# Kernel optimization log

Hardware: AMD Instinct MI355X
Metric: run time of the kernel (lower is better)

## Reference

```python
import jax, jax.numpy as jnp
import numpy as np


def _conv(x, w, b, pad):
    o = jax.lax.conv_general_dilated(x, w, (1, 1), [(pad, pad), (pad, pad)],
                                     dimension_numbers=('NCHW', 'OIHW', 'NCHW'))
    return o + b[None, :, None, None]


def _prelu(x, a):
    return jnp.where(x >= 0, x, a * x)


def _bn(x, g, b):
    # training-mode BatchNorm2d (biased variance, eps=1e-5)
    m = jnp.mean(x, axis=(0, 2, 3), keepdims=True)
    v = jnp.var(x, axis=(0, 2, 3), keepdims=True)
    return (x - m) * jax.lax.rsqrt(v + 1e-5) * g[None, :, None, None] + b[None, :, None, None]


def _maxpool2(x):
    return jax.lax.reduce_window(x, -jnp.inf, jax.lax.max, (1, 1, 2, 2), (1, 1, 2, 2), 'VALID')


def _up2(x):
    # bilinear upsample x2, align_corners=True
    B, C, H, W = x.shape
    Ho, Wo = 2 * H, 2 * W
    ys = jnp.arange(Ho, dtype=x.dtype) * ((H - 1) / (Ho - 1))
    xs = jnp.arange(Wo, dtype=x.dtype) * ((W - 1) / (Wo - 1))
    y0 = jnp.floor(ys).astype(jnp.int32)
    y1 = jnp.minimum(y0 + 1, H - 1)
    wy = (ys - y0.astype(x.dtype))[:, None]
    x0 = jnp.floor(xs).astype(jnp.int32)
    x1 = jnp.minimum(x0 + 1, W - 1)
    wx = xs - x0.astype(x.dtype)
    rows = x[:, :, y0, :] * (1 - wy) + x[:, :, y1, :] * wy  # [B,C,Ho,W]
    return rows[:, :, :, x0] * (1 - wx) + rows[:, :, :, x1] * wx


def _dyn_conv(x, w):
    # per-sample dynamic conv: x [B,1,H,W], w [B,Cout,k,k], pad = k//2 - 1
    # fused as a single grouped conv (groups = B) instead of B*Cout tiny launches
    B, Cout, k, _ = w.shape
    pad = k // 2 - 1
    xi = x.reshape(1, B, x.shape[2], x.shape[3])
    wi = w.reshape(B * Cout, 1, k, k)
    o = jax.lax.conv_general_dilated(xi, wi, (1, 1), [(pad, pad), (pad, pad)],
                                     dimension_numbers=('NCHW', 'OIHW', 'NCHW'),
                                     feature_group_count=B)
    return o.reshape(B, Cout, o.shape[2], o.shape[3])


def _double(x, w1, b1, w2, b2, a1, a2):
    return _prelu(_conv(_prelu(_conv(x, w1, b1, 1), a1), w2, b2, 1), a2)


def _forward(x, w, c1_w, c1_b, d2_w1, d2_b1, d2_w2, d2_b2, d3_w1, d3_b1, d3_w2, d3_b2,
             d4_w1, d4_b1, d4_w2, d4_b2, u3_w1, u3_b1, u3_w2, u3_b2, u2_w1, u2_b1,
             u2_w2, u2_b2, u1_w1, u1_b1, u1_w2, u1_b2, last_w, last_b,
             bn1_g, bn1_b, bn2_g, bn2_b, bn3_g, bn3_b, bn4_g, bn4_b, prelu_a):
    c1 = _prelu(_dyn_conv(x, w), prelu_a[0])          # [B,32,H-1,W-1]
    c1 = _prelu(_conv(c1, c1_w, c1_b, 2), prelu_a[1])  # 4x4 pad 2 -> [B,32,H,W]
    c1 = _bn(c1, bn1_g, bn1_b)
    h = _maxpool2(c1)
    c2 = _bn(_double(h, d2_w1, d2_b1, d2_w2, d2_b2, prelu_a[2], prelu_a[3]), bn2_g, bn2_b)
    h = _maxpool2(c2)
    c3 = _bn(_double(h, d3_w1, d3_b1, d3_w2, d3_b2, prelu_a[4], prelu_a[5]), bn3_g, bn3_b)
    h = _maxpool2(c3)
    h = _bn(_double(h, d4_w1, d4_b1, d4_w2, d4_b2, prelu_a[6], prelu_a[7]), bn4_g, bn4_b)
    h = jnp.concatenate([_up2(h), c3], axis=1)  # 512+256
    h = _double(h, u3_w1, u3_b1, u3_w2, u3_b2, prelu_a[8], prelu_a[9])
    h = jnp.concatenate([_up2(h), c2], axis=1)  # 256+128
    h = _double(h, u2_w1, u2_b1, u2_w2, u2_b2, prelu_a[10], prelu_a[11])
    h = jnp.concatenate([_up2(h), c1], axis=1)  # 128+32
    h = _double(h, u1_w1, u1_b1, u1_w2, u1_b2, prelu_a[12], prelu_a[13])
    return _conv(h, last_w, last_b, 0)


def setup_inputs() -> dict:
    key = jax.random.key(0)
    ks = iter(jax.random.split(key, 32))
    d = {}
    d['x'] = jax.random.normal(next(ks), (8, 1, 256, 256), jnp.float32)
    d['w'] = jax.random.normal(next(ks), (8, 32, 8, 8), jnp.float32) * 0.1
    wspecs = [('c1_w', (32, 32, 4, 4)), ('d2_w1', (128, 32, 3, 3)), ('d2_w2', (128, 128, 3, 3)),
              ('d3_w1', (256, 128, 3, 3)), ('d3_w2', (256, 256, 3, 3)),
              ('d4_w1', (512, 256, 3, 3)), ('d4_w2', (512, 512, 3, 3)),
              ('u3_w1', (256, 768, 3, 3)), ('u3_w2', (256, 256, 3, 3)),
              ('u2_w1', (128, 384, 3, 3)), ('u2_w2', (128, 128, 3, 3)),
              ('u1_w1', (32, 160, 3, 3)), ('u1_w2', (32, 32, 3, 3)), ('last_w', (1, 32, 1, 1))]
    for name, shp in wspecs:
        d[name] = jax.random.normal(next(ks), shp, jnp.float32) * 0.05
        d[name.replace('_w', '_b')] = jnp.zeros((shp[0],), jnp.float32)
    for name, c in [('bn1', 32), ('bn2', 128), ('bn3', 256), ('bn4', 512)]:
        d[name + '_g'] = jnp.ones((c,), jnp.float32)
        d[name + '_b'] = jnp.zeros((c,), jnp.float32)
    d['prelu_a'] = jnp.full((14,), 0.25, jnp.float32)
    return d


def reference(x, w, c1_w, c1_b, d2_w1, d2_b1, d2_w2, d2_b2, d3_w1, d3_b1, d3_w2, d3_b2,
              d4_w1, d4_b1, d4_w2, d4_b2, u3_w1, u3_b1, u3_w2, u3_b2, u2_w1, u2_b1,
              u2_w2, u2_b2, u1_w1, u1_b1, u1_w2, u1_b2, last_w, last_b,
              bn1_g, bn1_b, bn2_g, bn2_b, bn3_g, bn3_b, bn4_g, bn4_b, prelu_a):
    return _forward(x, w, c1_w, c1_b, d2_w1, d2_b1, d2_w2, d2_b2, d3_w1, d3_b1,
                    d3_w2, d3_b2, d4_w1, d4_b1, d4_w2, d4_b2, u3_w1, u3_b1, u3_w2,
                    u3_b2, u2_w1, u2_b1, u2_w2, u2_b2, u1_w1, u1_b1, u1_w2, u1_b2,
                    last_w, last_b, bn1_g, bn1_b, bn2_g, bn2_b, bn3_g, bn3_b,
                    bn4_g, bn4_b, prelu_a)
```

## Files before the change

kernel.cpp:

```cpp
#include <hip/hip_runtime.h>
#include <hip/hip_bf16.h>
#include <cstddef>


typedef _Float16 h16;
typedef __attribute__((ext_vector_type(8))) _Float16 h16x8;
typedef __attribute__((ext_vector_type(4))) float f32x4;
union F8 { uint4 u; h16x8 h; };
union UH { unsigned u; h16 h[2]; };

__device__ __forceinline__ float h2f(unsigned short s) {
    union { h16 h; unsigned short s; } c; c.s = s; return (float)c.h;
}
__device__ __forceinline__ unsigned short f2h(float f) {
    union { h16 h; unsigned short s; } c; c.h = (h16)f; return c.s;
}
__device__ __forceinline__ unsigned pack2(float a, float b) {
    return (unsigned)f2h(a) | ((unsigned)f2h(b) << 16);
}
__device__ __forceinline__ void up8(const uint4& v, float* f) {
    f[0]=h2f(v.x&0xffff); f[1]=h2f(v.x>>16);
    f[2]=h2f(v.y&0xffff); f[3]=h2f(v.y>>16);
    f[4]=h2f(v.z&0xffff); f[5]=h2f(v.z>>16);
    f[6]=h2f(v.w&0xffff); f[7]=h2f(v.w>>16);
}

__global__ void k_pack(const float* __restrict__ w, h16* __restrict__ pw,
                       int I, int T, int OB)
{
    int i8 = blockIdx.x * 64 + threadIdx.x;
    if (i8 >= (I >> 3)) return;
    int t = blockIdx.y, o = blockIdx.z;
    int ob = o / OB, om = o - ob * OB;
    int mt = om >> 4, m16 = om & 15;
    int chunk = i8 >> 2, quad = i8 & 3;
    int lane = quad * 16 + m16;
    int nch = I >> 5;
    size_t grp = ((((size_t)ob * T + t) * nch + chunk) * (OB >> 4) + mt) * 64 + lane;
    const float* src = w + ((size_t)o * I + i8 * 8) * T + t;
    h16* d = pw + grp * 8;
#pragma unroll
    for (int j = 0; j < 8; ++j) d[j] = (h16)src[(size_t)j * T];
}

template<int KH, int KW, int PAD, bool UPS, int MT>
__global__ __launch_bounds__(256, 2) void k_conv_mfma(
    const h16* __restrict__ src1, int C1n, int H1, int W1,
    const h16* __restrict__ src2, int C2n,
    int Hin, int Win, int Ho, int Wo,
    const h16* __restrict__ PW, const float* __restrict__ bias,
    const float* __restrict__ pa, int aidx,
    h16* __restrict__ out, int Cout)
{
    constexpr int WINH = 8 + KH - 1, WINW = 32 + KW - 1;
    constexpr int NPIX = WINH * WINW;
    constexpr int NIT  = NPIX * 4;
    constexpr int MAXIT = (NIT + 255) / 256;
    constexpr int TAPS = KH * KW;
    __shared__ unsigned short lds[2][NPIX * 36];

    const int tid = threadIdx.x;
    const int lane = tid & 63, wv = tid >> 6;
    const int quad = lane >> 4, m16 = lane & 15;
    const int nCb = Cout / (16 * MT);
    const int b  = blockIdx.z / nCb, cb = blockIdx.z % nCb;
    const int x0 = blockIdx.x * 32, y0 = blockIdx.y * 8;
    const int Cin = C1n + C2n;
    const int nch = Cin >> 5;
    const int co_base = cb * (16 * MT);
    const int srcH = UPS ? Hin : H1;
    const int srcW = UPS ? Win : W1;

    int lof[MAXIT];
    int g1[MAXIT];
    int fl[MAXIT];
    unsigned fyfx[MAXIT];
    int g2[MAXIT];

    const float ry = UPS ? (float)(H1 - 1) / (float)(Hin - 1) : 0.f;
    const float rx = UPS ? (float)(W1 - 1) / (float)(Win - 1) : 0.f;
    const int W1C = UPS ? W1 * C1n : 0;

#pragma unroll
    for (int it = 0; it < MAXIT; ++it) {
        int i = tid + it * 256;
        if (i >= NIT) { lof[it] = -1; g1[it] = -1; g2[it] = -1; fl[it] = 0; fyfx[it] = 0; continue; }
        int p = i >> 2, q = i & 3;
        int wy = p / WINW, wx = p - wy * WINW;
        int yy = y0 - PAD + wy, xx = x0 - PAD + wx;
        lof[it] = p * 36 + q * 8;
        bool val = (unsigned)yy < (unsigned)srcH && (unsigned)xx < (unsigned)srcW;
        if (UPS) {
            fl[it] = 0; fyfx[it] = 0; g1[it] = -1; g2[it] = -1;
            if (val) {
                float ys = yy * ry, xs = xx * rx;
                int yl0 = (int)ys, xl0 = (int)xs;
                float fy = ys - (float)yl0, fx = xs - (float)xl0;
                g1[it] = ((b * H1 + yl0) * W1 + xl0) * C1n + q * 8;
                fl[it] = (yl0 < H1 - 1 ? 1 : 0) | (xl0 < W1 - 1 ? 2 : 0);
                fyfx[it] = pack2(fy, fx);
                g2[it] = ((b * Hin + yy) * Win + xx) * C2n + q * 8;
            }
        } else {
            fl[it] = 0; fyfx[it] = 0; g2[it] = -1;
            g1[it] = val ? ((b * H1 + yy) * W1 + xx) * C1n + q * 8 : -1;
        }
    }

    f32x4 acc[MT][4];
#pragma unroll
    for (int i = 0; i < MT; ++i)
#pragma unroll
        for (int j = 0; j < 4; ++j) acc[i][j] = (f32x4){0.f, 0.f, 0.f, 0.f};

    auto stage = [&](int c0, unsigned short* buf) {
        if (UPS && c0 < C1n) {
#pragma unroll
            for (int it = 0; it < MAXIT; ++it) {
                int lo = lof[it];
                if (lo < 0) continue;
                uint2 lo8 = {0u, 0u}, hi8 = {0u, 0u};
                int g = g1[it];
                if (g >= 0) {
                    const h16* p00 = src1 + g + c0;
                    int oy = (fl[it] & 1) ? W1C : 0;
                    int ox = (fl[it] & 2) ? C1n : 0;
                    F8 v00, v01, v10, v11;
                    v00.u = *(const uint4*)(p00);
                    v01.u = *(const uint4*)(p00 + ox);
                    v10.u = *(const uint4*)(p00 + oy);
                    v11.u = *(const uint4*)(p00 + oy + ox);
                    UH t; t.u = fyfx[it];
                    h16 fy = t.h[0], fx = t.h[1];
                    h16x8 r0 = v00.h + (v10.h - v00.h) * fy;
                    h16x8 r1 = v01.h + (v11.h - v01.h) * fy;
                    F8 rr; rr.h = r0 + (r1 - r0) * fx;
                    lo8 = make_uint2(rr.u.x, rr.u.y);
                    hi8 = make_uint2(rr.u.z, rr.u.w);
                }
                *(uint2*)&buf[lo] = lo8;
                *(uint2*)&buf[lo + 4] = hi8;
            }
        } else if (UPS) {
            int cs = c0 - C1n;
#pragma unroll
            for (int it = 0; it < MAXIT; ++it) {
                int lo = lof[it];
                if (lo < 0) continue;
                uint4 v = {0u, 0u, 0u, 0u};
                int g = g2[it];
                if (g >= 0) v = *(const uint4*)(src2 + g + cs);
                *(uint2*)&buf[lo] = make_uint2(v.x, v.y);
                *(uint2*)&buf[lo + 4] = make_uint2(v.z, v.w);
            }
        } else {
#pragma unroll
            for (int it = 0; it < MAXIT; ++it) {
                int lo = lof[it];
                if (lo < 0) continue;
                uint4 v = {0u, 0u, 0u, 0u};
                int g = g1[it];
                if (g >= 0) v = *(const uint4*)(src1 + g + c0);
                *(uint2*)&buf[lo] = make_uint2(v.x, v.y);
                *(uint2*)&buf[lo + 4] = make_uint2(v.z, v.w);
            }
        }
    };

    const uint4* PW4 = (const uint4*)PW;
    auto sweep = [&](int ci, const unsigned short* buf) {
        size_t abase = (((size_t)cb * TAPS) * nch + ci) * (MT * 64) + lane;
        const size_t astep = (size_t)nch * (MT * 64);
#pragma unroll
        for (int kx = 0; kx < KW; ++kx) {
            F8 a[KH][MT];
#pragma unroll
            for (int ky = 0; ky < KH; ++ky)
#pragma unroll
                for (int mt = 0; mt < MT; ++mt)
                    a[ky][mt].u = PW4[abase + (size_t)(ky * KW + kx) * astep + mt * 64];
#pragma unroll
            for (int wr = 0; wr < 2 + KH - 1; ++wr) {
#pragma unroll
                for (int cg = 0; cg < 2; ++cg) {
                    int row = (wv << 1) + wr;
                    int col = (cg << 4) + m16;
                    int li = (row * WINW + col + kx) * 36 + quad * 8;
                    F8 bf;
                    ((uint2*)&bf)[0] = *(const uint2*)&buf[li];
                    ((uint2*)&bf)[1] = *(const uint2*)&buf[li + 4];
#pragma unroll
                    for (int ky = 0; ky < KH; ++ky) {
                        int ntr = wr - ky;
                        if (ntr < 0 || ntr > 1) continue;
                        int nt = (ntr << 1) + cg;
#pragma unroll
                        for (int mt = 0; mt < MT; ++mt)
                            acc[mt][nt] = __builtin_amdgcn_mfma_f32_16x16x32_f16(
                                a[ky][mt].h, bf.h, acc[mt][nt], 0, 0, 0);
                    }
                }
            }
        }
    };

    stage(0, lds[0]);
    __syncthreads();
    for (int ci = 0; ci < nch; ++ci) {
        int p = ci & 1;
        if (ci + 1 < nch) stage((ci + 1) << 5, lds[p ^ 1]);
        sweep(ci, lds[p]);
        __syncthreads();
    }

    const float alpha = pa[aidx];
#pragma unroll
    for (int mt = 0; mt < MT; ++mt) {
        int co = co_base + mt * 16 + quad * 4;
        float4 bi = *(const float4*)(bias + co);
#pragma unroll
        for (int nt = 0; nt < 4; ++nt) {
            int y = y0 + (wv << 1) + (nt >> 1);
            int x = x0 + ((nt & 1) << 4) + m16;
            float v0 = acc[mt][nt][0] + bi.x;
            float v1 = acc[mt][nt][1] + bi.y;
            float v2 = acc[mt][nt][2] + bi.z;
            float v3 = acc[mt][nt][3] + bi.w;
            v0 = v0 >= 0.f ? v0 : alpha * v0;
            v1 = v1 >= 0.f ? v1 : alpha * v1;
            v2 = v2 >= 0.f ? v2 : alpha * v2;
            v3 = v3 >= 0.f ? v3 : alpha * v3;
            uint2 r; r.x = pack2(v0, v1); r.y = pack2(v2, v3);
            *(uint2*)(out + ((size_t)((b * Ho + y) * Wo + x)) * Cout + co) = r;
        }
    }
}

__global__ __launch_bounds__(256) void k_dynconv(
    const float* __restrict__ x,
    const float* __restrict__ w,
    const float* __restrict__ pa,
    h16* __restrict__ out)
{
    __shared__ float wl[2048];
    int b = blockIdx.y;
    for (int j = threadIdx.x; j < 2048; j += 256) {
        int t = j >> 5, co = j & 31;
        wl[j] = w[((size_t)(b * 32 + co)) * 64 + t];
    }
    __syncthreads();
    int idx = blockIdx.x * 256 + threadIdx.x;
    if (idx >= 65025) return;
    int py = idx / 255, px = idx - py * 255;
    float acc[32];
#pragma unroll
    for (int c = 0; c < 32; ++c) acc[c] = 0.f;
    const float* xp = x + (size_t)b * 65536;
#pragma unroll
    for (int ky = 0; ky < 8; ++ky) {
        int iy = py + ky - 3;
        if ((unsigned)iy >= 256u) continue;
        const float* row = xp + iy * 256;
#pragma unroll
        for (int kx = 0; kx < 8; ++kx) {
            int ix = px + kx - 3;
            if ((unsigned)ix >= 256u) continue;
            float v = row[ix];
            const float4* wr = (const float4*)&wl[(ky * 8 + kx) * 32];
#pragma unroll
            for (int cg = 0; cg < 8; ++cg) {
                float4 wv = wr[cg];
                acc[cg*4+0] += v * wv.x; acc[cg*4+1] += v * wv.y;
                acc[cg*4+2] += v * wv.z; acc[cg*4+3] += v * wv.w;
            }
        }
    }
    float a = pa[0];
    h16* op = out + ((size_t)(b * 65025 + idx)) * 32;
#pragma unroll
    for (int cg = 0; cg < 4; ++cg) {
        float v[8];
#pragma unroll
        for (int k = 0; k < 8; ++k) {
            float t = acc[cg * 8 + k];
            v[k] = t >= 0.f ? t : a * t;
        }
        uint4 r;
        r.x = pack2(v[0], v[1]); r.y = pack2(v[2], v[3]);
        r.z = pack2(v[4], v[5]); r.w = pack2(v[6], v[7]);
        *(uint4*)(op + cg * 8) = r;
    }
}

__global__ __launch_bounds__(256) void k_pool(
    const h16* __restrict__ in, h16* __restrict__ out,
    int Hin, int Win, int C, int lc8, int lwo, int count)
{
    int idx = blockIdx.x * 256 + threadIdx.x;
    if (idx >= count) return;
    int b = blockIdx.y;
    int c8 = idx & ((1 << lc8) - 1);
    int t  = idx >> lc8;
    int ox = t & ((1 << lwo) - 1);
    int oy = t >> lwo;
    const h16* p = in + ((size_t)((b * Hin + oy * 2) * Win + ox * 2)) * C + c8 * 8;
    uint4 v00 = *(const uint4*)p;
    uint4 v01 = *(const uint4*)(p + C);
    uint4 v10 = *(const uint4*)(p + (size_t)Win * C);
    uint4 v11 = *(const uint4*)(p + (size_t)Win * C + C);
    float a[8], bb[8], c[8], d[8];
    up8(v00, a); up8(v01, bb); up8(v10, c); up8(v11, d);
    uint4 r;
    float m[8];
#pragma unroll
    for (int k = 0; k < 8; ++k) m[k] = fmaxf(fmaxf(a[k], bb[k]), fmaxf(c[k], d[k]));
    r.x = pack2(m[0], m[1]); r.y = pack2(m[2], m[3]);
    r.z = pack2(m[4], m[5]); r.w = pack2(m[6], m[7]);
    int Wo = 1 << lwo;
    *(uint4*)(out + ((size_t)((b * (Hin >> 1) + oy) * Wo + ox)) * C + c8 * 8) = r;
}

__global__ __launch_bounds__(256) void k_bnstats(
    const h16* __restrict__ x, int C, int N, float* __restrict__ sums)
{
    __shared__ float ls[1024];
    for (int j = threadIdx.x; j < 2 * C; j += 256) ls[j] = 0.f;
    __syncthreads();
    int start = blockIdx.x * 256 + threadIdx.x;
    int stride = gridDim.x * 256;
    int c = start & (C - 1);
    float s = 0.f, q = 0.f;
    for (int i = start; i < N; i += stride) {
        float v = h2f(((const unsigned short*)x)[i]);
        s += v; q += v * v;
    }
    atomicAdd(&ls[c], s);
    atomicAdd(&ls[C + c], q);
    __syncthreads();
    for (int j = threadIdx.x; j < 2 * C; j += 256) atomicAdd(&sums[j], ls[j]);
}

__global__ void k_bnfin(
    const float* __restrict__ sums, const float* __restrict__ g,
    const float* __restrict__ bta, int C, float invN, float* __restrict__ sc)
{
    int c = threadIdx.x;
    if (c >= C) return;
    float mean = sums[c] * invN;
    float var  = sums[C + c] * invN - mean * mean;
    float s    = g[c] / sqrtf(var + 1e-5f);
    sc[c]      = s;
    sc[C + c]  = bta[c] - mean * s;
}

__global__ __launch_bounds__(256) void k_bnapply(
    h16* __restrict__ x, int C, int N8, const float* __restrict__ sc)
{
    __shared__ float ls[1024];
    for (int j = threadIdx.x; j < 2 * C; j += 256) ls[j] = sc[j];
    __syncthreads();
    int idx = blockIdx.x * 256 + threadIdx.x;
    if (idx >= N8) return;
    int cb = (idx << 3) & (C - 1);
    h16* p = x + (size_t)idx * 8;
    uint4 v = *(const uint4*)p;
    float f[8];
    up8(v, f);
    uint4 r;
    float o[8];
#pragma unroll
    for (int k = 0; k < 8; ++k) o[k] = f[k] * ls[cb + k] + ls[C + cb + k];
    r.x = pack2(o[0], o[1]); r.y = pack2(o[2], o[3]);
    r.z = pack2(o[4], o[5]); r.w = pack2(o[6], o[7]);
    *(uint4*)p = r;
}

__global__ __launch_bounds__(256) void k_final(
    const h16* __restrict__ in, const float* __restrict__ w,
    const float* __restrict__ bias, float* __restrict__ out)
{
    int idx = blockIdx.x * 256 + threadIdx.x;
    if (idx >= 524288) return;
    const h16* p = in + (size_t)idx * 32;
    float acc = bias[0];
#pragma unroll
    for (int cg = 0; cg < 4; ++cg) {
        uint4 v = *(const uint4*)(p + cg * 8);
        float f[8];
        up8(v, f);
#pragma unroll
        for (int k = 0; k < 8; ++k) acc += f[k] * w[cg * 8 + k];
    }
    out[idx] = acc;
}

extern "C" void kernel_launch(void* const* d_in, const int* in_sizes, int n_in,
                              void* d_out, int out_size, void* d_ws, size_t ws_size,
                              hipStream_t stream)
{
    const float* x      = (const float*)d_in[0];
    const float* w      = (const float*)d_in[1];
    const float* c1_w   = (const float*)d_in[2];
    const float* c1_b   = (const float*)d_in[3];
    const float* d2_w1  = (const float*)d_in[4];
    const float* d2_b1  = (const float*)d_in[5];
    const float* d2_w2  = (const float*)d_in[6];
    const float* d2_b2  = (const float*)d_in[7];
    const float* d3_w1  = (const float*)d_in[8];
    const float* d3_b1  = (const float*)d_in[9];
    const float* d3_w2  = (const float*)d_in[10];
    const float* d3_b2  = (const float*)d_in[11];
    const float* d4_w1  = (const float*)d_in[12];
    const float* d4_b1  = (const float*)d_in[13];
    const float* d4_w2  = (const float*)d_in[14];
    const float* d4_b2  = (const float*)d_in[15];
    const float* u3_w1  = (const float*)d_in[16];
    const float* u3_b1  = (const float*)d_in[17];
    const float* u3_w2  = (const float*)d_in[18];
    const float* u3_b2  = (const float*)d_in[19];
    const float* u2_w1  = (const float*)d_in[20];
    const float* u2_b1  = (const float*)d_in[21];
    const float* u2_w2  = (const float*)d_in[22];
    const float* u2_b2  = (const float*)d_in[23];
    const float* u1_w1  = (const float*)d_in[24];
    const float* u1_b1  = (const float*)d_in[25];
    const float* u1_w2  = (const float*)d_in[26];
    const float* u1_b2  = (const float*)d_in[27];
    const float* last_w = (const float*)d_in[28];
    const float* last_b = (const float*)d_in[29];
    const float* bn1_g  = (const float*)d_in[30];
    const float* bn1_b  = (const float*)d_in[31];
    const float* bn2_g  = (const float*)d_in[32];
    const float* bn2_b  = (const float*)d_in[33];
    const float* bn3_g  = (const float*)d_in[34];
    const float* bn3_b  = (const float*)d_in[35];
    const float* bn4_g  = (const float*)d_in[36];
    const float* bn4_b  = (const float*)d_in[37];
    const float* pa     = (const float*)d_in[38];
    float* out = (float*)d_out;

    h16* A0 = (h16*)d_ws;
    h16* C1 = A0;
    h16* C2 = A0 + 16777216;
    h16* C3 = A0 + 33554432;
    h16* A  = A0 + 41943040;
    h16* B  = A0 + 58720256;
    h16* PWb= A0 + 75497472;
    float* SUMS = (float*)(A0 + 83126272);
    float* SC   = SUMS + 1024;
    size_t need = (size_t)83126272 * 2 + 8192;
    if (ws_size < need) return;

    h16* pw_c1   = PWb;
    h16* pw_d2w1 = PWb + 16384;
    h16* pw_d2w2 = PWb + 53248;
    h16* pw_d3w1 = PWb + 200704;
    h16* pw_d3w2 = PWb + 495616;
    h16* pw_d4w1 = PWb + 1085440;
    h16* pw_d4w2 = PWb + 2265088;
    h16* pw_u3w1 = PWb + 4624384;
    h16* pw_u3w2 = PWb + 6393856;
    h16* pw_u2w1 = PWb + 6983680;
    h16* pw_u2w2 = PWb + 7426048;
    h16* pw_u1w1 = PWb + 7573504;
    h16* pw_u1w2 = PWb + 7619584;

    dim3 blk(256);

    auto pack = [&](const float* src, h16* dst, int I, int T, int O, int OB) {
        k_pack<<<dim3(((I >> 3) + 63) / 64, T, O), 64, 0, stream>>>(src, dst, I, T, OB);
    };
    pack(c1_w,  pw_c1,   32, 16, 32, 32);
    pack(d2_w1, pw_d2w1, 32,  9, 128, 64);
    pack(d2_w2, pw_d2w2, 128, 9, 128, 64);
    pack(d3_w1, pw_d3w1, 128, 9, 256, 64);
    pack(d3_w2, pw_d3w2, 256, 9, 256, 64);
    pack(d4_w1, pw_d4w1, 256, 9, 512, 64);
    pack(d4_w2, pw_d4w2, 512, 9, 512, 64);
    pack(u3_w1, pw_u3w1, 768, 9, 256, 64);
    pack(u3_w2, pw_u3w2, 256, 9, 256, 64);
    pack(u2_w1, pw_u2w1, 384, 9, 128, 64);
    pack(u2_w2, pw_u2w2, 128, 9, 128, 64);
    pack(u1_w1, pw_u1w1, 160, 9, 32, 32);
    pack(u1_w2, pw_u1w2, 32,  9, 32, 32);

    auto bn = [&](h16* buf, int C, int N, const float* g, const float* bb) {
        hipMemsetAsync(SUMS, 0, 2 * C * sizeof(float), stream);
        k_bnstats<<<dim3(1024), blk, 0, stream>>>(buf, C, N, SUMS);
        k_bnfin<<<dim3(1), dim3(512), 0, stream>>>(SUMS, g, bb, C, (float)C / (float)N, SC);
        k_bnapply<<<dim3(N / 8 / 256), blk, 0, stream>>>(buf, C, N / 8, SC);
    };

    k_dynconv<<<dim3(255, 8), blk, 0, stream>>>(x, w, pa, A);
    k_conv_mfma<4,4,2,false,2><<<dim3(8, 32, 8), blk, 0, stream>>>(
        A, 32, 255, 255, nullptr, 0, 255, 255, 256, 256,
        pw_c1, c1_b, pa, 1, C1, 32);
    bn(C1, 32, 16777216, bn1_g, bn1_b);
    k_pool<<<dim3(256, 8), blk, 0, stream>>>(C1, B, 256, 256, 32, 2, 7, 65536);

    k_conv_mfma<3,3,1,false,4><<<dim3(4, 16, 16), blk, 0, stream>>>(
        B, 32, 128, 128, nullptr, 0, 128, 128, 128, 128,
        pw_d2w1, d2_b1, pa, 2, A, 128);
    k_conv_mfma<3,3,1,false,4><<<dim3(4, 16, 16), blk, 0, stream>>>(
        A, 128, 128, 128, nullptr, 0, 128, 128, 128, 128,
        pw_d2w2, d2_b2, pa, 3, C2, 128);
    bn(C2, 128, 16777216, bn2_g, bn2_b);
    k_pool<<<dim3(256, 8), blk, 0, stream>>>(C2, B, 128, 128, 128, 4, 6, 65536);

    k_conv_mfma<3,3,1,false,4><<<dim3(2, 8, 32), blk, 0, stream>>>(
        B, 128, 64, 64, nullptr, 0, 64, 64, 64, 64,
        pw_d3w1, d3_b1, pa, 4, A, 256);
    k_conv_mfma<3,3,1,false,4><<<dim3(2, 8, 32), blk, 0, stream>>>(
        A, 256, 64, 64, nullptr, 0, 64, 64, 64, 64,
        pw_d3w2, d3_b2, pa, 5, C3, 256);
    bn(C3, 256, 8388608, bn3_g, bn3_b);
    k_pool<<<dim3(128, 8), blk, 0, stream>>>(C3, B, 64, 64, 256, 5, 5, 32768);

    k_conv_mfma<3,3,1,false,4><<<dim3(1, 4, 64), blk, 0, stream>>>(
        B, 256, 32, 32, nullptr, 0, 32, 32, 32, 32,
        pw_d4w1, d4_b1, pa, 6, A, 512);
    k_conv_mfma<3,3,1,false,4><<<dim3(1, 4, 64), blk, 0, stream>>>(
        A, 512, 32, 32, nullptr, 0, 32, 32, 32, 32,
        pw_d4w2, d4_b2, pa, 7, B, 512);
    bn(B, 512, 4194304, bn4_g, bn4_b);

    k_conv_mfma<3,3,1,true,4><<<dim3(2, 8, 32), blk, 0, stream>>>(
        B, 512, 32, 32, C3, 256, 64, 64, 64, 64,
        pw_u3w1, u3_b1, pa, 8, A, 256);
    k_conv_mfma<3,3,1,false,4><<<dim3(2, 8, 32), blk, 0, stream>>>(
        A, 256, 64, 64, nullptr, 0, 64, 64, 64, 64,
        pw_u3w2, u3_b2, pa, 9, B, 256);

    k_conv_mfma<3,3,1,true,4><<<dim3(4, 16, 16), blk, 0, stream>>>(
        B, 256, 64, 64, C2, 128, 128, 128, 128, 128,
        pw_u2w1, u2_b1, pa, 10, A, 128);
    k_conv_mfma<3,3,1,false,4><<<dim3(4, 16, 16), blk, 0, stream>>>(
        A, 128, 128, 128, nullptr, 0, 128, 128, 128, 128,
        pw_u2w2, u2_b2, pa, 11, B, 128);

    k_conv_mfma<3,3,1,true,2><<<dim3(8, 32, 8), blk, 0, stream>>>(
        B, 128, 128, 128, C1, 32, 256, 256, 256, 256,
        pw_u1w1, u1_b1, pa, 12, A, 32);
    k_conv_mfma<3,3,1,false,2><<<dim3(8, 32, 8), blk, 0, stream>>>(
        A, 32, 256, 256, nullptr, 0, 256, 256, 256, 256,
        pw_u1w2, u1_b2, pa, 13, B, 32);

    k_final<<<dim3(2048), blk, 0, stream>>>(B, last_w, last_b, out);
}
```

Measured before the change: 1.221 ms.

## Fuse BN apply with maxpool, final 1x1 into last conv, batch weight packing

```diff
diff --git a/kernel.cpp b/kernel.cpp
--- a/kernel.cpp
+++ b/kernel.cpp
@@ -25,32 +25,43 @@
     f[6]=h2f(v.w&0xffff); f[7]=h2f(v.w>>16);
 }
 
-__global__ void k_pack(const float* __restrict__ w, h16* __restrict__ pw,
-                       int I, int T, int OB)
-{
-    int i8 = blockIdx.x * 64 + threadIdx.x;
-    if (i8 >= (I >> 3)) return;
-    int t = blockIdx.y, o = blockIdx.z;
-    int ob = o / OB, om = o - ob * OB;
+struct PackDesc { const float* src; h16* dst; int I, T, OB, nGrp; };
+struct PackArgs { PackDesc d[13]; int total; };
+
+__global__ __launch_bounds__(256) void k_packall(PackArgs a)
+{
+    int gid = blockIdx.x * 256 + threadIdx.x;
+    if (gid >= a.total) return;
+    int li = 0, rel = gid;
+    while (rel >= a.d[li].nGrp) { rel -= a.d[li].nGrp; ++li; }
+    const PackDesc& D = a.d[li];
+    int I8 = D.I >> 3;
+    int o  = rel / (D.T * I8);
+    int r2 = rel - o * (D.T * I8);
+    int t  = r2 / I8;
+    int i8 = r2 - t * I8;
+    int ob = o / D.OB, om = o - ob * D.OB;
     int mt = om >> 4, m16 = om & 15;
     int chunk = i8 >> 2, quad = i8 & 3;
     int lane = quad * 16 + m16;
-    int nch = I >> 5;
-    size_t grp = ((((size_t)ob * T + t) * nch + chunk) * (OB >> 4) + mt) * 64 + lane;
-    const float* src = w + ((size_t)o * I + i8 * 8) * T + t;
-    h16* d = pw + grp * 8;
-#pragma unroll
-    for (int j = 0; j < 8; ++j) d[j] = (h16)src[(size_t)j * T];
-}
-
-template<int KH, int KW, int PAD, bool UPS, int MT>
+    int nch = D.I >> 5;
+    size_t grp = ((((size_t)ob * D.T + t) * nch + chunk) * (D.OB >> 4) + mt) * 64 + lane;
+    const float* src = D.src + ((size_t)o * D.I + i8 * 8) * D.T + t;
+    h16* d = D.dst + grp * 8;
+#pragma unroll
+    for (int j = 0; j < 8; ++j) d[j] = (h16)src[(size_t)j * D.T];
+}
+
+template<int KH, int KW, int PAD, bool UPS, int MT, bool FIN>
 __global__ __launch_bounds__(256, 2) void k_conv_mfma(
     const h16* __restrict__ src1, int C1n, int H1, int W1,
     const h16* __restrict__ src2, int C2n,
     int Hin, int Win, int Ho, int Wo,
     const h16* __restrict__ PW, const float* __restrict__ bias,
     const float* __restrict__ pa, int aidx,
-    h16* __restrict__ out, int Cout)
+    h16* __restrict__ out, int Cout,
+    const float* __restrict__ fw, const float* __restrict__ fb,
+    float* __restrict__ fout)
 {
     constexpr int WINH = 8 + KH - 1, WINW = 32 + KW - 1;
     constexpr int NPIX = WINH * WINW;
@@ -214,10 +225,13 @@
     }
 
     const float alpha = pa[aidx];
+    float fin_acc[4] = {0.f, 0.f, 0.f, 0.f};
 #pragma unroll
     for (int mt = 0; mt < MT; ++mt) {
         int co = co_base + mt * 16 + quad * 4;
         float4 bi = *(const float4*)(bias + co);
+        float4 fw4 = {0.f, 0.f, 0.f, 0.f};
+        if (FIN) fw4 = *(const float4*)(fw + co);
 #pragma unroll
         for (int nt = 0; nt < 4; ++nt) {
             int y = y0 + (wv << 1) + (nt >> 1);
@@ -230,8 +244,26 @@
             v1 = v1 >= 0.f ? v1 : alpha * v1;
             v2 = v2 >= 0.f ? v2 : alpha * v2;
             v3 = v3 >= 0.f ? v3 : alpha * v3;
-            uint2 r; r.x = pack2(v0, v1); r.y = pack2(v2, v3);
-            *(uint2*)(out + ((size_t)((b * Ho + y) * Wo + x)) * Cout + co) = r;
+            if (FIN) {
+                fin_acc[nt] += v0 * fw4.x + v1 * fw4.y + v2 * fw4.z + v3 * fw4.w;
+            } else {
+                uint2 r; r.x = pack2(v0, v1); r.y = pack2(v2, v3);
+                *(uint2*)(out + ((size_t)((b * Ho + y) * Wo + x)) * Cout + co) = r;
+            }
+        }
+    }
+    if (FIN) {
+        float fb0 = fb[0];
+#pragma unroll
+        for (int nt = 0; nt < 4; ++nt) {
+            float p = fin_acc[nt];
+            p += __shfl_xor(p, 16);
+            p += __shfl_xor(p, 32);
+            if (quad == 0) {
+                int y = y0 + (wv << 1) + (nt >> 1);
+                int x = x0 + ((nt & 1) << 4) + m16;
+                fout[(size_t)(b * Ho + y) * Wo + x] = p + fb0;
+            }
         }
     }
 }
@@ -290,34 +322,6 @@
         r.z = pack2(v[4], v[5]); r.w = pack2(v[6], v[7]);
         *(uint4*)(op + cg * 8) = r;
     }
-}
-
-__global__ __launch_bounds__(256) void k_pool(
-    const h16* __restrict__ in, h16* __restrict__ out,
-    int Hin, int Win, int C, int lc8, int lwo, int count)
-{
-    int idx = blockIdx.x * 256 + threadIdx.x;
-    if (idx >= count) return;
-    int b = blockIdx.y;
-    int c8 = idx & ((1 << lc8) - 1);
-    int t  = idx >> lc8;
-    int ox = t & ((1 << lwo) - 1);
-    int oy = t >> lwo;
-    const h16* p = in + ((size_t)((b * Hin + oy * 2) * Win + ox * 2)) * C + c8 * 8;
-    uint4 v00 = *(const uint4*)p;
-    uint4 v01 = *(const uint4*)(p + C);
-    uint4 v10 = *(const uint4*)(p + (size_t)Win * C);
-    uint4 v11 = *(const uint4*)(p + (size_t)Win * C + C);
-    float a[8], bb[8], c[8], d[8];
-    up8(v00, a); up8(v01, bb); up8(v10, c); up8(v11, d);
-    uint4 r;
-    float m[8];
-#pragma unroll
-    for (int k = 0; k < 8; ++k) m[k] = fmaxf(fmaxf(a[k], bb[k]), fmaxf(c[k], d[k]));
-    r.x = pack2(m[0], m[1]); r.y = pack2(m[2], m[3]);
-    r.z = pack2(m[4], m[5]); r.w = pack2(m[6], m[7]);
-    int Wo = 1 << lwo;
-    *(uint4*)(out + ((size_t)((b * (Hin >> 1) + oy) * Wo + ox)) * C + c8 * 8) = r;
 }
 
 __global__ __launch_bounds__(256) void k_bnstats(
@@ -351,6 +355,52 @@
     float s    = g[c] / sqrtf(var + 1e-5f);
     sc[c]      = s;
     sc[C + c]  = bta[c] - mean * s;
+}
+
+__global__ __launch_bounds__(256) void k_bnapply_pool(
+    h16* __restrict__ x, h16* __restrict__ pooled,
+    int Hin, int Win, int C, int lc8, int lwo, int count,
+    const float* __restrict__ sc)
+{
+    int idx = blockIdx.x * 256 + threadIdx.x;
+    if (idx >= count) return;
+    int b = blockIdx.y;
+    int c8 = idx & ((1 << lc8) - 1);
+    int t  = idx >> lc8;
+    int ox = t & ((1 << lwo) - 1);
+    int oy = t >> lwo;
+    int cb = c8 * 8;
+    float s[8], sh[8];
+#pragma unroll
+    for (int k = 0; k < 8; ++k) { s[k] = sc[cb + k]; sh[k] = sc[C + cb + k]; }
+    h16* p = x + ((size_t)((b * Hin + oy * 2) * Win + ox * 2)) * C + cb;
+    size_t rs = (size_t)Win * C;
+    uint4 v00 = *(const uint4*)p;
+    uint4 v01 = *(const uint4*)(p + C);
+    uint4 v10 = *(const uint4*)(p + rs);
+    uint4 v11 = *(const uint4*)(p + rs + C);
+    float a[8], bb[8], c[8], d[8], m[8];
+    up8(v00, a); up8(v01, bb); up8(v10, c); up8(v11, d);
+#pragma unroll
+    for (int k = 0; k < 8; ++k) {
+        a[k]  = a[k]  * s[k] + sh[k];
+        bb[k] = bb[k] * s[k] + sh[k];
+        c[k]  = c[k]  * s[k] + sh[k];
+        d[k]  = d[k]  * s[k] + sh[k];
+        m[k]  = fmaxf(fmaxf(a[k], bb[k]), fmaxf(c[k], d[k]));
+    }
+    uint4 r;
+    r.x = pack2(a[0],a[1]);  r.y = pack2(a[2],a[3]);  r.z = pack2(a[4],a[5]);  r.w = pack2(a[6],a[7]);
+    *(uint4*)p = r;
+    r.x = pack2(bb[0],bb[1]); r.y = pack2(bb[2],bb[3]); r.z = pack2(bb[4],bb[5]); r.w = pack2(bb[6],bb[7]);
+    *(uint4*)(p + C) = r;
+    r.x = pack2(c[0],c[1]);  r.y = pack2(c[2],c[3]);  r.z = pack2(c[4],c[5]);  r.w = pack2(c[6],c[7]);
+    *(uint4*)(p + rs) = r;
+    r.x = pack2(d[0],d[1]);  r.y = pack2(d[2],d[3]);  r.z = pack2(d[4],d[5]);  r.w = pack2(d[6],d[7]);
+    *(uint4*)(p + rs + C) = r;
+    r.x = pack2(m[0],m[1]);  r.y = pack2(m[2],m[3]);  r.z = pack2(m[4],m[5]);  r.w = pack2(m[6],m[7]);
+    int Wo = 1 << lwo;
+    *(uint4*)(pooled + ((size_t)((b * (Hin >> 1) + oy)) * Wo + ox) * C + cb) = r;
 }
 
 __global__ __launch_bounds__(256) void k_bnapply(
@@ -373,25 +423,6 @@
     r.x = pack2(o[0], o[1]); r.y = pack2(o[2], o[3]);
     r.z = pack2(o[4], o[5]); r.w = pack2(o[6], o[7]);
     *(uint4*)p = r;
-}
-
-__global__ __launch_bounds__(256) void k_final(
-    const h16* __restrict__ in, const float* __restrict__ w,
-    const float* __restrict__ bias, float* __restrict__ out)
-{
-    int idx = blockIdx.x * 256 + threadIdx.x;
-    if (idx >= 524288) return;
-    const h16* p = in + (size_t)idx * 32;
-    float acc = bias[0];
-#pragma unroll
-    for (int cg = 0; cg < 4; ++cg) {
-        uint4 v = *(const uint4*)(p + cg * 8);
-        float f[8];
-        up8(v, f);
-#pragma unroll
-        for (int k = 0; k < 8; ++k) acc += f[k] * w[cg * 8 + k];
-    }
-    out[idx] = acc;
 }
 
 extern "C" void kernel_launch(void* const* d_in, const int* in_sizes, int n_in,
@@ -447,8 +478,8 @@
     h16* B  = A0 + 58720256;
     h16* PWb= A0 + 75497472;
     float* SUMS = (float*)(A0 + 83126272);
-    float* SC   = SUMS + 1024;
-    size_t need = (size_t)83126272 * 2 + 8192;
+    float* SC   = SUMS + 2048;
+    size_t need = (size_t)83126272 * 2 + 3072 * 4;
     if (ws_size < need) return;
 
     h16* pw_c1   = PWb;
@@ -467,83 +498,88 @@
 
     dim3 blk(256);
 
-    auto pack = [&](const float* src, h16* dst, int I, int T, int O, int OB) {
-        k_pack<<<dim3(((I >> 3) + 63) / 64, T, O), 64, 0, stream>>>(src, dst, I, T, OB);
+    hipMemsetAsync(SUMS, 0, 2048 * sizeof(float), stream);
+
+    PackArgs pk;
+    auto mk = [](const float* s, h16* d, int I, int T, int O, int OB) {
+        return PackDesc{s, d, I, T, OB, (I >> 3) * T * O};
     };
-    pack(c1_w,  pw_c1,   32, 16, 32, 32);
-    pack(d2_w1, pw_d2w1, 32,  9, 128, 64);
-    pack(d2_w2, pw_d2w2, 128, 9, 128, 64);
-    pack(d3_w1, pw_d3w1, 128, 9, 256, 64);
-    pack(d3_w2, pw_d3w2, 256, 9, 256, 64);
-    pack(d4_w1, pw_d4w1, 256, 9, 512, 64);
-    pack(d4_w2, pw_d4w2, 512, 9, 512, 64);
-    pack(u3_w1, pw_u3w1, 768, 9, 256, 64);
-    pack(u3_w2, pw_u3w2, 256, 9, 256, 64);
-    pack(u2_w1, pw_u2w1, 384, 9, 128, 64);
-    pack(u2_w2, pw_u2w2, 128, 9, 128, 64);
-    pack(u1_w1, pw_u1w1, 160, 9, 32, 32);
-    pack(u1_w2, pw_u1w2, 32,  9, 32, 32);
-
-    auto bn = [&](h16* buf, int C, int N, const float* g, const float* bb) {
-        hipMemsetAsync(SUMS, 0, 2 * C * sizeof(float), stream);
-        k_bnstats<<<dim3(1024), blk, 0, stream>>>(buf, C, N, SUMS);
-        k_bnfin<<<dim3(1), dim3(512), 0, stream>>>(SUMS, g, bb, C, (float)C / (float)N, SC);
-        k_bnapply<<<dim3(N / 8 / 256), blk, 0, stream>>>(buf, C, N / 8, SC);
-    };
+    pk.d[0]  = mk(c1_w,  pw_c1,   32, 16, 32, 32);
+    pk.d[1]  = mk(d2_w1, pw_d2w1, 32,  9, 128, 64);
+    pk.d[2]  = mk(d2_w2, pw_d2w2, 128, 9, 128, 64);
+    pk.d[3]  = mk(d3_w1, pw_d3w1, 128, 9, 256, 64);
+    pk.d[4]  = mk(d3_w2, pw_d3w2, 256, 9, 256, 64);
+    pk.d[5]  = mk(d4_w1, pw_d4w1, 256, 9, 512, 32);
+    pk.d[6]  = mk(d4_w2, pw_d4w2, 512, 9, 512, 32);
+    pk.d[7]  = mk(u3_w1, pw_u3w1, 768, 9, 256, 64);
+    pk.d[8]  = mk(u3_w2, pw_u3w2, 256, 9, 256, 64);
+    pk.d[9]  = mk(u2_w1, pw_u2w1, 384, 9, 128, 64);
+    pk.d[10] = mk(u2_w2, pw_u2w2, 128, 9, 128, 64);
+    pk.d[11] = mk(u1_w1, pw_u1w1, 160, 9, 32, 32);
+    pk.d[12] = mk(u1_w2, pw_u1w2, 32,  9, 32, 32);
+    pk.total = 0;
+    for (int i = 0; i < 13; ++i) pk.total += pk.d[i].nGrp;
+    k_packall<<<dim3((pk.total + 255) / 256), blk, 0, stream>>>(pk);
+
+    const float* NF = nullptr;
+    float* NFO = nullptr;
 
     k_dynconv<<<dim3(255, 8), blk, 0, stream>>>(x, w, pa, A);
-    k_conv_mfma<4,4,2,false,2><<<dim3(8, 32, 8), blk, 0, stream>>>(
+    k_conv_mfma<4,4,2,false,2,false><<<dim3(8, 32, 8), blk, 0, stream>>>(
         A, 32, 255, 255, nullptr, 0, 255, 255, 256, 256,
-        pw_c1, c1_b, pa, 1, C1, 32);
-    bn(C1, 32, 16777216, bn1_g, bn1_b);
-    k_pool<<<dim3(256, 8), blk, 0, stream>>>(C1, B, 256, 256, 32, 2, 7, 65536);
-
-    k_conv_mfma<3,3,1,false,4><<<dim3(4, 16, 16), blk, 0, stream>>>(
+        pw_c1, c1_b, pa, 1, C1, 32, NF, NF, NFO);
+    k_bnstats<<<dim3(1024), blk, 0, stream>>>(C1, 32, 16777216, SUMS);
+    k_bnfin<<<dim3(1), dim3(512), 0, stream>>>(SUMS, bn1_g, bn1_b, 32, 32.f / 16777216.f, SC);
+    k_bnapply_pool<<<dim3(256, 8), blk, 0, stream>>>(C1, B, 256, 256, 32, 2, 7, 65536, SC);
+
+    k_conv_mfma<3,3,1,false,4,false><<<dim3(4, 16, 16), blk, 0, stream>>>(
         B, 32, 128, 128, nullptr, 0, 128, 128, 128, 128,
-        pw_d2w1, d2_b1, pa, 2, A, 128);
-    k_conv_mfma<3,3,1,false,4><<<dim3(4, 16, 16), blk, 0, stream>>>(
+        pw_d2w1, d2_b1, pa, 2, A, 128, NF, NF, NFO);
+    k_conv_mfma<3,3,1,false,4,false><<<dim3(4, 16, 16), blk, 0, stream>>>(
         A, 128, 128, 128, nullptr, 0, 128, 128, 128, 128,
-        pw_d2w2, d2_b2, pa, 3, C2, 128);
-    bn(C2, 128, 16777216, bn2_g, bn2_b);
-    k_pool<<<dim3(256, 8), blk, 0, stream>>>(C2, B, 128, 128, 128, 4, 6, 65536);
-
-    k_conv_mfma<3,3,1,false,4><<<dim3(2, 8, 32), blk, 0, stream>>>(
+        pw_d2w2, d2_b2, pa, 3, C2, 128, NF, NF, NFO);
+    k_bnstats<<<dim3(1024), blk, 0, stream>>>(C2, 128, 16777216, SUMS + 64);
+    k_bnfin<<<dim3(1), dim3(512), 0, stream>>>(SUMS + 64, bn2_g, bn2_b, 128, 128.f / 16777216.f, SC);
+    k_bnapply_pool<<<dim3(256, 8), blk, 0, stream>>>(C2, B, 128, 128, 128, 4, 6, 65536, SC);
+
+    k_conv_mfma<3,3,1,false,4,false><<<dim3(2, 8, 32), blk, 0, stream>>>(
         B, 128, 64, 64, nullptr, 0, 64, 64, 64, 64,
-        pw_d3w1, d3_b1, pa, 4, A, 256);
-    k_conv_mfma<3,3,1,false,4><<<dim3(2, 8, 32), blk, 0, stream>>>(
+        pw_d3w1, d3_b1, pa, 4, A, 256, NF, NF, NFO);
+    k_conv_mfma<3,3,1,false,4,false><<<dim3(2, 8, 32), blk, 0, stream>>>(
         A, 256, 64, 64, nullptr, 0, 64, 64, 64, 64,
-        pw_d3w2, d3_b2, pa, 5, C3, 256);
-    bn(C3, 256, 8388608, bn3_g, bn3_b);
-    k_pool<<<dim3(128, 8), blk, 0, stream>>>(C3, B, 64, 64, 256, 5, 5, 32768);
-
-    k_conv_mfma<3,3,1,false,4><<<dim3(1, 4, 64), blk, 0, stream>>>(
+        pw_d3w2, d3_b2, pa, 5, C3, 256, NF, NF, NFO);
+    k_bnstats<<<dim3(1024), blk, 0, stream>>>(C3, 256, 8388608, SUMS + 320);
+    k_bnfin<<<dim3(1), dim3(512), 0, stream>>>(SUMS + 320, bn3_g, bn3_b, 256, 256.f / 8388608.f, SC);
+    k_bnapply_pool<<<dim3(128, 8), blk, 0, stream>>>(C3, B, 64, 64, 256, 5, 5, 32768, SC);
+
+    k_conv_mfma<3,3,1,false,2,false><<<dim3(1, 4, 128), blk, 0, stream>>>(
         B, 256, 32, 32, nullptr, 0, 32, 32, 32, 32,
-        pw_d4w1, d4_b1, pa, 6, A, 512);
-    k_conv_mfma<3,3,1,false,4><<<dim3(1, 4, 64), blk, 0, stream>>>(
+        pw_d4w1, d4_b1, pa, 6, A, 512, NF, NF, NFO);
+    k_conv_mfma<3,3,1,false,2,false><<<dim3(1, 4, 128), blk, 0, stream>>>(
         A, 512, 32, 32, nullptr, 0, 32, 32, 32, 32,
-        pw_d4w2, d4_b2, pa, 7, B, 512);
-    bn(B, 512, 4194304, bn4_g, bn4_b);
-
-    k_conv_mfma<3,3,1,true,4><<<dim3(2, 8, 32), blk, 0, stream>>>(
+        pw_d4w2, d4_b2, pa, 7, B, 512, NF, NF, NFO);
+    k_bnstats<<<dim3(1024), blk, 0, stream>>>(B, 512, 4194304, SUMS + 832);
+    k_bnfin<<<dim3(1), dim3(512), 0, stream>>>(SUMS + 832, bn4_g, bn4_b, 512, 512.f / 4194304.f, SC);
+    k_bnapply<<<dim3(2048), blk, 0, stream>>>(B, 512, 524288, SC);
+
+    k_conv_mfma<3,3,1,true,4,false><<<dim3(2, 8, 32), blk, 0, stream>>>(
         B, 512, 32, 32, C3, 256, 64, 64, 64, 64,
-        pw_u3w1, u3_b1, pa, 8, A, 256);
-    k_conv_mfma<3,3,1,false,4><<<dim3(2, 8, 32), blk, 0, stream>>>(
+        pw_u3w1, u3_b1, pa, 8, A, 256, NF, NF, NFO);
+    k_conv_mfma<3,3,1,false,4,false><<<dim3(2, 8, 32), blk, 0, stream>>>(
         A, 256, 64, 64, nullptr, 0, 64, 64, 64, 64,
-        pw_u3w2, u3_b2, pa, 9, B, 256);
-
-    k_conv_mfma<3,3,1,true,4><<<dim3(4, 16, 16), blk, 0, stream>>>(
+        pw_u3w2, u3_b2, pa, 9, B, 256, NF, NF, NFO);
+
+    k_conv_mfma<3,3,1,true,4,false><<<dim3(4, 16, 16), blk, 0, stream>>>(
         B, 256, 64, 64, C2, 128, 128, 128, 128, 128,
-        pw_u2w1, u2_b1, pa, 10, A, 128);
-    k_conv_mfma<3,3,1,false,4><<<dim3(4, 16, 16), blk, 0, stream>>>(
+        pw_u2w1, u2_b1, pa, 10, A, 128, NF, NF, NFO);
+    k_conv_mfma<3,3,1,false,4,false><<<dim3(4, 16, 16), blk, 0, stream>>>(
         A, 128, 128, 128, nullptr, 0, 128, 128, 128, 128,
-        pw_u2w2, u2_b2, pa, 11, B, 128);
-
-    k_conv_mfma<3,3,1,true,2><<<dim3(8, 32, 8), blk, 0, stream>>>(
+        pw_u2w2, u2_b2, pa, 11, B, 128, NF, NF, NFO);
+
+    k_conv_mfma<3,3,1,true,2,false><<<dim3(8, 32, 8), blk, 0, stream>>>(
         B, 128, 128, 128, C1, 32, 256, 256, 256, 256,
-        pw_u1w1, u1_b1, pa, 12, A, 32);
-    k_conv_mfma<3,3,1,false,2><<<dim3(8, 32, 8), blk, 0, stream>>>(
+        pw_u1w1, u1_b1, pa, 12, A, 32, NF, NF, NFO);
+    k_conv_mfma<3,3,1,false,2,true><<<dim3(8, 32, 8), blk, 0, stream>>>(
         A, 32, 256, 256, nullptr, 0, 256, 256, 256, 256,
-        pw_u1w2, u1_b2, pa, 13, B, 32);
-
-    k_final<<<dim3(2048), blk, 0, stream>>>(B, last_w, last_b, out);
-}
+        pw_u1w2, u1_b2, pa, 13, B, 32, last_w, last_b, out);
+}
```

New measurement: 1.186 ms. 1.03x faster.
